# Kernel optimization log

Hardware: AMD Instinct MI355X
Metric: run time of the kernel (lower is better)

## Reference

```python
import jax, jax.numpy as jnp
import numpy as np

WINDOW = 512  # sliding-window size (keys per query, including self)


def setup_inputs() -> dict:
    key = jax.random.key(0)
    ks = jax.random.split(key, 5)
    B, T, C = 2, 8192, 1024
    s = 1.0 / np.sqrt(C)
    return {
        "x": jax.random.normal(ks[0], (B, T, C), dtype=jnp.float32),
        "Wq": jax.random.normal(ks[1], (C, C), dtype=jnp.float32) * s,
        "Wk": jax.random.normal(ks[2], (C, C), dtype=jnp.float32) * s,
        "Wv": jax.random.normal(ks[3], (C, C), dtype=jnp.float32) * s,
        "Wo": jax.random.normal(ks[4], (C, C), dtype=jnp.float32) * s,
    }


def _block_local_attn(q, k, v, window):
    # q,k,v: [B,H,T,D]; causal sliding-window attention, honoring sparsity by
    # attending only to the current and previous block of size `window`.
    B, H, T, D = q.shape
    W = window
    nb = T // W
    scale = 1.0 / jnp.sqrt(jnp.asarray(D, q.dtype))
    qb = q.reshape(B, H, nb, W, D)
    kb = k.reshape(B, H, nb, W, D)
    vb = v.reshape(B, H, nb, W, D)
    # previous block (zero-padded for block 0)
    kp = jnp.pad(kb, ((0, 0), (0, 0), (1, 0), (0, 0), (0, 0)))[:, :, :nb]
    vp = jnp.pad(vb, ((0, 0), (0, 0), (1, 0), (0, 0), (0, 0)))[:, :, :nb]
    k2 = jnp.concatenate([kp, kb], axis=3)  # [B,H,nb,2W,D]
    v2 = jnp.concatenate([vp, vb], axis=3)
    i = jnp.arange(W)[:, None]          # query index within block
    j = jnp.arange(2 * W)[None, :]      # key index (0..W-1 prev, W..2W-1 cur)
    # key global offset = j - W relative to query block start; causal window of
    # size W (self + W-1 previous) <=> i < j <= i + W
    base = (j > i) & (j <= i + W)                                  # [W,2W]
    prev_ok = (jnp.arange(nb)[:, None] > 0) | (jnp.arange(2 * W)[None, :] >= W)
    mask = base[None, :, :] & prev_ok[:, None, :]                  # [nb,W,2W]
    scores = jnp.einsum("bhnqd,bhnkd->bhnqk", qb, k2) * scale
    scores = jnp.where(mask[None, None], scores, jnp.asarray(-1e30, scores.dtype))
    p = jax.nn.softmax(scores, axis=-1)
    out = jnp.einsum("bhnqk,bhnkd->bhnqd", p, v2)
    return out.reshape(B, H, T, D)


def reference(x, Wq, Wk, Wv, Wo):
    B, T, C = x.shape
    H = 16
    D = C // H
    # nn.Linear(y = x @ W^T), bias=False
    q = (x @ Wq.T).reshape(B, T, H, D).transpose(0, 2, 1, 3)
    k = (x @ Wk.T).reshape(B, T, H, D).transpose(0, 2, 1, 3)
    v = (x @ Wv.T).reshape(B, T, H, D).transpose(0, 2, 1, 3)
    out = _block_local_attn(q, k, v, WINDOW)
    out = out.transpose(0, 2, 1, 3).reshape(B, T, C)
    return out @ Wo.T
```

## Files before the change

kernel.cpp:

```cpp
#include <hip/hip_runtime.h>
#include <hip/hip_bf16.h>
#include <stdint.h>

typedef __attribute__((ext_vector_type(8))) short short8;
typedef __attribute__((ext_vector_type(4))) float f32x4;
typedef __hip_bfloat16 bf16;

#define AS1 __attribute__((address_space(1)))
#define AS3 __attribute__((address_space(3)))

__device__ __forceinline__ void gl16(const void* g, void* l) {
  __builtin_amdgcn_global_load_lds((const AS1 unsigned int*)g,
                                   (AS3 unsigned int*)l, 16, 0, 0);
}

__device__ __forceinline__ unsigned short bfbits(float x) {
  union { bf16 b; unsigned short u; } c; c.b = __float2bfloat16(x); return c.u;
}

#define SCHED0 __builtin_amdgcn_sched_barrier(0)

__global__ __launch_bounds__(256) void k_cvt(const float* __restrict__ src,
                                             bf16* __restrict__ dst, int n8) {
  int i = blockIdx.x * blockDim.x + threadIdx.x;
  int stride = gridDim.x * blockDim.x;
  for (; i < n8; i += stride) {
    const float4* p = (const float4*)src + (size_t)i * 2;
    float4 a = p[0], b = p[1];
    bf16 tmp[8];
    tmp[0] = __float2bfloat16(a.x); tmp[1] = __float2bfloat16(a.y);
    tmp[2] = __float2bfloat16(a.z); tmp[3] = __float2bfloat16(a.w);
    tmp[4] = __float2bfloat16(b.x); tmp[5] = __float2bfloat16(b.y);
    tmp[6] = __float2bfloat16(b.z); tmp[7] = __float2bfloat16(b.w);
    *(short8*)(dst + (size_t)i * 8) = *(short8*)tmp;
  }
}


#define GEMM_BODY(...)                                                         \
  const int Kd = 1024;                                                         \
  const int nk = 32;                                              \
  __shared__ bf16 As[4][256 * 32];                                             \
  __shared__ bf16 Bs[4][256 * 32];                                             \
  int tid = threadIdx.x;                                                       \
  int lane = tid & 63, wid = tid >> 6;                                         \
  int l15 = lane & 15, hi = lane >> 4;                                         \
  int wm = wid >> 2, wn = wid & 3;                                             \
  f32x4 acc[8][4];                                                             \
  _Pragma("unroll") for (int i = 0; i < 8; i++)                                \
      _Pragma("unroll") for (int j = 0; j < 4; j++)                            \
          acc[i][j] = (f32x4){0.f, 0.f, 0.f, 0.f};                             \
  auto stageA = [&](int slot, int kk) {                                        \
    const bf16* ab = Abase + kk * 32;                                          \
    _Pragma("unroll") for (int pass = 0; pass < 2; pass++) {                   \
      int p = pass * 512 + tid;                                                \
      int row = p >> 2;                                                        \
      int u = (p & 3) ^ ((row >> 1) & 3);                                      \
      gl16(ab + (size_t)row * Kd + u * 8, (char*)(&As[slot][0]) + p * 16);     \
    }                                                                          \
  };                                                                           \
  auto stageB = [&](int slot, int kk) {                                        \
    const bf16* bb = Bbase + kk * 32;                                          \
    _Pragma("unroll") for (int pass = 0; pass < 2; pass++) {                   \
      int p = pass * 512 + tid;                                                \
      int row = p >> 2;                                                        \
      int u = (p & 3) ^ ((row >> 1) & 3);                                      \
      gl16(bb + (size_t)row * Kd + u * 8, (char*)(&Bs[slot][0]) + p * 16);     \
    }                                                                          \
  };                                                                           \
  stageA(0, 0); stageB(0, 0);                                                  \
  stageA(1, 1); stageB(1, 1);                                                  \
  stageA(2, 2); stageB(2, 2);                                                  \
  asm volatile("s_waitcnt vmcnt(8)" ::: "memory");                             \
  SCHED0; __builtin_amdgcn_s_barrier(); SCHED0;                                \
  int sw = ((l15 >> 1) & 3) << 4;                                              \
  for (int t = 0; t < nk; ++t) {                                               \
    int slot = t & 3;                                                          \
    const char* Ab = (const char*)(&As[slot][0]);                              \
    const char* Bb = (const char*)(&Bs[slot][0]);                              \
             \
    if (t + 3 < nk) stageA((t + 3) & 3, t + 3);                                \
    short8 afr[4], bfr[4];                                                     \
    _Pragma("unroll") for (int mf = 0; mf < 4; mf++) {                         \
      int row = wm * 128 + mf * 16 + l15;                                      \
      afr[mf] = *(const short8*)(Ab + ((row * 64 + hi * 16) ^ sw));            \
    }                                                                          \
    _Pragma("unroll") for (int nf = 0; nf < 4; nf++) {                         \
      int row = wn * 64 + nf * 16 + l15;                                       \
      bfr[nf] = *(const short8*)(Bb + ((row * 64 + hi * 16) ^ sw));            \
    }                                                                          \
    SCHED0; __builtin_amdgcn_s_barrier(); SCHED0;                              \
    __builtin_amdgcn_s_setprio(1);                                             \
    _Pragma("unroll") for (int mf = 0; mf < 4; mf++)                           \
        _Pragma("unroll") for (int nf = 0; nf < 4; nf++)                       \
            acc[mf][nf] = __builtin_amdgcn_mfma_f32_16x16x32_bf16(             \
                afr[mf], bfr[nf], acc[mf][nf], 0, 0, 0);                       \
    __builtin_amdgcn_s_setprio(0);                                             \
    SCHED0; __builtin_amdgcn_s_barrier(); SCHED0;                              \
                  \
    if (t + 3 < nk) stageB((t + 3) & 3, t + 3);                                \
    short8 afr2[4];                                                            \
    _Pragma("unroll") for (int mf = 0; mf < 4; mf++) {                         \
      int row = wm * 128 + 64 + mf * 16 + l15;                                 \
      afr2[mf] = *(const short8*)(Ab + ((row * 64 + hi * 16) ^ sw));           \
    }                                                                          \
    SCHED0;                                                                    \
    if (t + 3 < nk)      asm volatile("s_waitcnt vmcnt(8)" ::: "memory");      \
    else if (t + 2 < nk) asm volatile("s_waitcnt vmcnt(4)" ::: "memory");      \
    else if (t + 1 < nk) asm volatile("s_waitcnt vmcnt(0)" ::: "memory");      \
    SCHED0; __builtin_amdgcn_s_barrier(); SCHED0;                              \
    __builtin_amdgcn_s_setprio(1);                                             \
    _Pragma("unroll") for (int mf = 0; mf < 4; mf++)                           \
        _Pragma("unroll") for (int nf = 0; nf < 4; nf++)                       \
            acc[mf + 4][nf] = __builtin_amdgcn_mfma_f32_16x16x32_bf16(         \
                afr2[mf], bfr[nf], acc[mf + 4][nf], 0, 0, 0);                  \
    __builtin_amdgcn_s_setprio(0);                                             \
    if (t + 1 < nk) { SCHED0; __builtin_amdgcn_s_barrier(); SCHED0; }          \
  }                                                                            \
  __VA_ARGS__

__global__ __launch_bounds__(512, 2) void k_qkv_gemm(
    const bf16* __restrict__ X, const bf16* __restrict__ Wq,
    const bf16* __restrict__ Wk, const bf16* __restrict__ Wv,
    bf16* __restrict__ Q, bf16* __restrict__ K, bf16* __restrict__ V) {
  int bid = blockIdx.x;
  int wsel = bid >> 8;
  int rem = bid & 255;
  int mt = rem & 63;
  int nt = rem >> 6;
  const bf16* W = (wsel == 0) ? Wq : (wsel == 1) ? Wk : Wv;
  bf16* Dst = (wsel == 0) ? Q : (wsel == 1) ? K : V;
  const bf16* Abase = X + (size_t)mt * 256 * 1024;
  const bf16* Bbase = W + (size_t)nt * 256 * 1024;
  GEMM_BODY({
    _Pragma("unroll") for (int mf = 0; mf < 8; mf++) {
      _Pragma("unroll") for (int r = 0; r < 4; r++) {
        int row = mt * 256 + wm * 128 + mf * 16 + hi * 4 + r;
        int b = row >> 13;
        int tok = row & 8191;
        _Pragma("unroll") for (int nf = 0; nf < 4; nf++) {
          int col = nt * 256 + wn * 64 + nf * 16 + l15;
          int h = col >> 6;
          int d = col & 63;
          Dst[((size_t)(b * 16 + h) * 8192 + tok) * 64 + d] =
              __float2bfloat16(acc[mf][nf][r]);
        }
      }
    }
  })
}

__global__ __launch_bounds__(512, 2) void k_out_gemm(
    const bf16* __restrict__ A, const bf16* __restrict__ Wo,
    float* __restrict__ Out) {
  int bid = blockIdx.x;
  int mt = bid & 63;
  int nt = bid >> 6;
  const bf16* Abase = A + (size_t)mt * 256 * 1024;
  const bf16* Bbase = Wo + (size_t)nt * 256 * 1024;
  GEMM_BODY({
    _Pragma("unroll") for (int mf = 0; mf < 8; mf++) {
      _Pragma("unroll") for (int r = 0; r < 4; r++) {
        int row = mt * 256 + wm * 128 + mf * 16 + hi * 4 + r;
        _Pragma("unroll") for (int nf = 0; nf < 4; nf++) {
          int col = nt * 256 + wn * 64 + nf * 16 + l15;
          Out[(size_t)row * 1024 + col] = acc[mf][nf][r];
        }
      }
    }
  })
}

__global__ __launch_bounds__(256) void k_vtrans(const bf16* __restrict__ V,
                                                bf16* __restrict__ VT) {
  const int T = 8192;
  __shared__ bf16 tile[64][72];
  int bid = blockIdx.x;
  int tb = bid & 127;
  int bh = bid >> 7;
  int t0 = tb * 64;
  int tid = threadIdx.x;
  int r = tid >> 2, c4 = tid & 3;
  const bf16* src = V + ((size_t)bh * T + t0 + r) * 64 + c4 * 16;
  short8 a = *(const short8*)src;
  short8 b2 = *(const short8*)(src + 8);
#pragma unroll
  for (int e = 0; e < 8; e++) tile[r][c4 * 16 + e] = ((bf16*)&a)[e];
#pragma unroll
  for (int e = 0; e < 8; e++) tile[r][c4 * 16 + 8 + e] = ((bf16*)&b2)[e];
  __syncthreads();
  alignas(16) bf16 o[16];
#pragma unroll
  for (int e = 0; e < 16; e++) o[e] = tile[c4 * 16 + e][r];
  bf16* dst = VT + ((size_t)bh * 64 + r) * T + t0 + c4 * 16;
  *(short8*)dst = *(short8*)o;
  *(short8*)(dst + 8) = *((short8*)o + 1);
}

__global__ __launch_bounds__(256) void k_attn(
    const bf16* __restrict__ Q, const bf16* __restrict__ K,
    const bf16* __restrict__ VT, bf16* __restrict__ ATT) {
  const int T = 8192;
  __shared__ bf16 Ks[2][64 * 64];
  __shared__ bf16 Vs[2][64 * 64];
  __shared__ bf16 Ps[4][16 * 64];
  int bid = blockIdx.x;
  int qt = bid & 127;
  int bh = bid >> 7;
  int b = bh >> 4, h = bh & 15;
  int tid = threadIdx.x;
  int lane = tid & 63, wid = tid >> 6;
  int l15 = lane & 15, hi = lane >> 4;
  int q0 = qt * 64;
  int qw = q0 + wid * 16;

  short8 bq[2];
  const bf16* qp = Q + ((size_t)bh * T + qw + l15) * 64 + hi * 8;
  bq[0] = *(const short8*)qp;
  bq[1] = *(const short8*)(qp + 32);

  const bf16* Kbh = K + (size_t)bh * T * 64;
  const bf16* Vbh = VT + (size_t)bh * 64 * T;

  auto stage = [&](int bb, int c0) {
#pragma unroll
    for (int pass = 0; pass < 2; pass++) {
      int p = pass * 256 + tid;
      int row = p >> 3;
      int u = (p & 7) ^ (row & 7);
      gl16(Kbh + ((size_t)(c0 + row)) * 64 + u * 8, (char*)(&Ks[bb][0]) + p * 16);
      gl16(Vbh + (size_t)row * T + c0 + u * 8, (char*)(&Vs[bb][0]) + p * 16);
    }
  };

  int cstart = q0 - 512; if (cstart < 0) cstart = 0;
  int nch = (q0 + 64 - cstart) >> 6;

  f32x4 oacc[4];
#pragma unroll
  for (int c = 0; c < 4; c++) oacc[c] = (f32x4){0.f, 0.f, 0.f, 0.f};
  float m = -1e30f, ssum = 0.f;

  stage(0, cstart);
  __syncthreads();
  int buf = 0;
  for (int ci = 0; ci < nch; ci++) {
    int c0 = cstart + (ci << 6);
    if (ci + 1 < nch) stage(buf ^ 1, c0 + 64);
    f32x4 sacc[4];
#pragma unroll
    for (int ks = 0; ks < 4; ks++) sacc[ks] = (f32x4){0.f, 0.f, 0.f, 0.f};
#pragma unroll
    for (int dh = 0; dh < 2; dh++) {
#pragma unroll
      for (int ks = 0; ks < 4; ks++) {
        int krow = ks * 16 + l15;
        int boff = ((krow * 64 + dh * 32 + hi * 8) * 2) ^ ((krow & 7) << 4);
        short8 ak = *(const short8*)((const char*)(&Ks[buf][0]) + boff);
        sacc[ks] = __builtin_amdgcn_mfma_f32_16x16x32_bf16(ak, bq[dh], sacc[ks], 0, 0, 0);
      }
    }
    int qg = qw + l15;
    float pv[4][4];
    float pmax = -1e30f;
#pragma unroll
    for (int ks = 0; ks < 4; ks++)
#pragma unroll
      for (int r = 0; r < 4; r++) {
        int jg = c0 + ks * 16 + hi * 4 + r;
        float s = sacc[ks][r] * 0.125f;
        bool ok = (jg <= qg) && (jg > qg - 512);
        s = ok ? s : -1e30f;
        pv[ks][r] = s;
        pmax = fmaxf(pmax, s);
      }
    pmax = fmaxf(pmax, __shfl_xor(pmax, 16));
    pmax = fmaxf(pmax, __shfl_xor(pmax, 32));
    float mnew = fmaxf(m, pmax);
    float corr = __expf(m - mnew);
    float psum = 0.f;
#pragma unroll
    for (int ks = 0; ks < 4; ks++)
#pragma unroll
      for (int r = 0; r < 4; r++) {
        float p = (pv[ks][r] > -1e29f) ? __expf(pv[ks][r] - mnew) : 0.f;
        pv[ks][r] = p;
        psum += p;
      }
    psum += __shfl_xor(psum, 16);
    psum += __shfl_xor(psum, 32);
    ssum = ssum * corr + psum;
    m = mnew;
#pragma unroll
    for (int r = 0; r < 4; r++) {
      float f = __shfl(corr, hi * 4 + r);
#pragma unroll
      for (int c = 0; c < 4; c++) oacc[c][r] *= f;
    }
#pragma unroll
    for (int ks = 0; ks < 4; ks++) {
      unsigned int lo = (unsigned)bfbits(pv[ks][0]) | ((unsigned)bfbits(pv[ks][1]) << 16);
      unsigned int hi2 = (unsigned)bfbits(pv[ks][2]) | ((unsigned)bfbits(pv[ks][3]) << 16);
      int j0 = ks * 16 + hi * 4;
      int a0 = ((l15 * 64 + j0) * 2) ^ ((l15 & 7) << 4);
      int a1 = ((l15 * 64 + j0 + 2) * 2) ^ ((l15 & 7) << 4);
      *(unsigned int*)((char*)(&Ps[wid][0]) + a0) = lo;
      *(unsigned int*)((char*)(&Ps[wid][0]) + a1) = hi2;
    }
    short8 ap[2];
#pragma unroll
    for (int js = 0; js < 2; js++) {
      int a = ((l15 * 64 + js * 32 + hi * 8) * 2) ^ ((l15 & 7) << 4);
      ap[js] = *(const short8*)((const char*)(&Ps[wid][0]) + a);
    }
#pragma unroll
    for (int js = 0; js < 2; js++)
#pragma unroll
      for (int c = 0; c < 4; c++) {
        int vrow = c * 16 + l15;
        int boff = ((vrow * 64 + js * 32 + hi * 8) * 2) ^ ((vrow & 7) << 4);
        short8 bv = *(const short8*)((const char*)(&Vs[buf][0]) + boff);
        oacc[c] = __builtin_amdgcn_mfma_f32_16x16x32_bf16(ap[js], bv, oacc[c], 0, 0, 0);
      }
    __syncthreads();
    buf ^= 1;
  }
  float inv = 1.f / ssum;
#pragma unroll
  for (int r = 0; r < 4; r++) {
    float f = __shfl(inv, hi * 4 + r);
    int tok = qw + hi * 4 + r;
    bf16* dst = ATT + ((size_t)b * 8192 + tok) * 1024 + h * 64;
#pragma unroll
    for (int c = 0; c < 4; c++)
      dst[c * 16 + l15] = __float2bfloat16(oacc[c][r] * f);
  }
}

extern "C" void kernel_launch(void* const* d_in, const int* in_sizes, int n_in,
                              void* d_out, int out_size, void* d_ws, size_t ws_size,
                              hipStream_t stream) {
  const float* x  = (const float*)d_in[0];
  const float* wq = (const float*)d_in[1];
  const float* wk = (const float*)d_in[2];
  const float* wv = (const float*)d_in[3];
  const float* wo = (const float*)d_in[4];
  float* out = (float*)d_out;

  char* ws = (char*)d_ws;
  const size_t SZ_X = (size_t)16384 * 1024 * 2;
  const size_t SZ_W = (size_t)1024 * 1024 * 2;
  size_t off = 0;
  bf16* xb  = (bf16*)(ws + off); off += SZ_X;
  bf16* wqb = (bf16*)(ws + off); off += SZ_W;
  bf16* wkb = (bf16*)(ws + off); off += SZ_W;
  bf16* wvb = (bf16*)(ws + off); off += SZ_W;
  bf16* wob = (bf16*)(ws + off); off += SZ_W;
  bf16* qb  = (bf16*)(ws + off); off += SZ_X;
  bf16* kb  = (bf16*)(ws + off); off += SZ_X;
  bf16* vb  = (bf16*)(ws + off); off += SZ_X;
  bf16* vtb = (bf16*)(ws + off); off += SZ_X;
  bf16* att = xb;

  k_cvt<<<2048, 256, 0, stream>>>(x, xb, 16384 * 1024 / 8);
  k_cvt<<<512, 256, 0, stream>>>(wq, wqb, 1024 * 1024 / 8);
  k_cvt<<<512, 256, 0, stream>>>(wk, wkb, 1024 * 1024 / 8);
  k_cvt<<<512, 256, 0, stream>>>(wv, wvb, 1024 * 1024 / 8);
  k_cvt<<<512, 256, 0, stream>>>(wo, wob, 1024 * 1024 / 8);
  k_qkv_gemm<<<768, 512, 0, stream>>>(xb, wqb, wkb, wvb, qb, kb, vb);
  k_vtrans<<<4096, 256, 0, stream>>>(vb, vtb);
  k_attn<<<4096, 256, 0, stream>>>(qb, kb, vtb, att);
  k_out_gemm<<<256, 512, 0, stream>>>(att, wob, out);
}
```

Baseline: 327.5 us.

## Software-pipeline LDS fragment loads in GEMM main loop, cut barriers per iteration

Restructures the GEMM k-loop so A and B fragments for the next k-step are read from LDS while the current step's second MFMA half is issued, with register double-buffering of the B fragments. The per-iteration barrier count drops from four to two, and the loop is unrolled by two. The aim is to hide LDS read latency behind MFMA work and cut synchronisation stalls. The cost is higher register pressure from the extra fragment buffers, which could hurt occupancy under launch_bounds(512,2). It also relies on subtle correctness of slot reuse with fewer barriers.

```diff
diff --git a/kernel.cpp b/kernel.cpp
--- a/kernel.cpp
+++ b/kernel.cpp
@@ -74,48 +74,58 @@
   asm volatile("s_waitcnt vmcnt(8)" ::: "memory");                             \
   SCHED0; __builtin_amdgcn_s_barrier(); SCHED0;                                \
   int sw = ((l15 >> 1) & 3) << 4;                                              \
-  for (int t = 0; t < nk; ++t) {                                               \
+  int arow0 = wm * 128 + l15;                                                  \
+  int brow0 = wn * 64 + l15;                                                   \
+  short8 a_cur[4], a_hi[4], b_cur[4], b_nxt[4];                                \
+  _Pragma("unroll") for (int mf = 0; mf < 4; mf++)                             \
+      a_cur[mf] = *(const short8*)((const char*)(&As[0][0]) +                  \
+                                   (((arow0 + mf * 16) * 64 + hi * 16) ^ sw)); \
+  _Pragma("unroll") for (int nf = 0; nf < 4; nf++)                             \
+      b_cur[nf] = *(const short8*)((const char*)(&Bs[0][0]) +                  \
+                                   (((brow0 + nf * 16) * 64 + hi * 16) ^ sw)); \
+  _Pragma("unroll 2") for (int t = 0; t < nk; ++t) {                           \
     int slot = t & 3;                                                          \
     const char* Ab = (const char*)(&As[slot][0]);                              \
-    const char* Bb = (const char*)(&Bs[slot][0]);                              \
              \
     if (t + 3 < nk) stageA((t + 3) & 3, t + 3);                                \
-    short8 afr[4], bfr[4];                                                     \
-    _Pragma("unroll") for (int mf = 0; mf < 4; mf++) {                         \
-      int row = wm * 128 + mf * 16 + l15;                                      \
-      afr[mf] = *(const short8*)(Ab + ((row * 64 + hi * 16) ^ sw));            \
-    }                                                                          \
-    _Pragma("unroll") for (int nf = 0; nf < 4; nf++) {                         \
-      int row = wn * 64 + nf * 16 + l15;                                       \
-      bfr[nf] = *(const short8*)(Bb + ((row * 64 + hi * 16) ^ sw));            \
-    }                                                                          \
-    SCHED0; __builtin_amdgcn_s_barrier(); SCHED0;                              \
+    _Pragma("unroll") for (int mf = 0; mf < 4; mf++)                           \
+        a_hi[mf] = *(const short8*)(Ab +                                       \
+            (((arow0 + 64 + mf * 16) * 64 + hi * 16) ^ sw));                   \
+    SCHED0;                                                                    \
     __builtin_amdgcn_s_setprio(1);                                             \
     _Pragma("unroll") for (int mf = 0; mf < 4; mf++)                           \
         _Pragma("unroll") for (int nf = 0; nf < 4; nf++)                       \
             acc[mf][nf] = __builtin_amdgcn_mfma_f32_16x16x32_bf16(             \
-                afr[mf], bfr[nf], acc[mf][nf], 0, 0, 0);                       \
+                a_cur[mf], b_cur[nf], acc[mf][nf], 0, 0, 0);                   \
     __builtin_amdgcn_s_setprio(0);                                             \
-    SCHED0; __builtin_amdgcn_s_barrier(); SCHED0;                              \
-                  \
+    SCHED0;                                                                    \
+      \
     if (t + 3 < nk) stageB((t + 3) & 3, t + 3);                                \
-    short8 afr2[4];                                                            \
-    _Pragma("unroll") for (int mf = 0; mf < 4; mf++) {                         \
-      int row = wm * 128 + 64 + mf * 16 + l15;                                 \
-      afr2[mf] = *(const short8*)(Ab + ((row * 64 + hi * 16) ^ sw));           \
+    if (t + 1 < nk) {                                                          \
+      SCHED0;                                                                  \
+      if (t + 3 < nk)      asm volatile("s_waitcnt vmcnt(8)" ::: "memory");    \
+      else if (t + 2 < nk) asm volatile("s_waitcnt vmcnt(4)" ::: "memory");    \
+      else                 asm volatile("s_waitcnt vmcnt(0)" ::: "memory");    \
+      SCHED0; __builtin_amdgcn_s_barrier(); SCHED0;                            \
+      const char* AbN = (const char*)(&As[(t + 1) & 3][0]);                    \
+      const char* BbN = (const char*)(&Bs[(t + 1) & 3][0]);                    \
+      _Pragma("unroll") for (int mf = 0; mf < 4; mf++)                         \
+          a_cur[mf] = *(const short8*)(AbN +                                   \
+              (((arow0 + mf * 16) * 64 + hi * 16) ^ sw));                      \
+      _Pragma("unroll") for (int nf = 0; nf < 4; nf++)                         \
+          b_nxt[nf] = *(const short8*)(BbN +                                   \
+              (((brow0 + nf * 16) * 64 + hi * 16) ^ sw));                      \
+      SCHED0;                                                                  \
     }                                                                          \
-    SCHED0;                                                                    \
-    if (t + 3 < nk)      asm volatile("s_waitcnt vmcnt(8)" ::: "memory");      \
-    else if (t + 2 < nk) asm volatile("s_waitcnt vmcnt(4)" ::: "memory");      \
-    else if (t + 1 < nk) asm volatile("s_waitcnt vmcnt(0)" ::: "memory");      \
-    SCHED0; __builtin_amdgcn_s_barrier(); SCHED0;                              \
     __builtin_amdgcn_s_setprio(1);                                             \
     _Pragma("unroll") for (int mf = 0; mf < 4; mf++)                           \
         _Pragma("unroll") for (int nf = 0; nf < 4; nf++)                       \
             acc[mf + 4][nf] = __builtin_amdgcn_mfma_f32_16x16x32_bf16(         \
-                afr2[mf], bfr[nf], acc[mf + 4][nf], 0, 0, 0);                  \
+                a_hi[mf], b_cur[nf], acc[mf + 4][nf], 0, 0, 0);                \
     __builtin_amdgcn_s_setprio(0);                                             \
-    if (t + 1 < nk) { SCHED0; __builtin_amdgcn_s_barrier(); SCHED0; }          \
+    SCHED0;                                                                    \
+    if (t + 1 < nk) { __builtin_amdgcn_s_barrier(); SCHED0; }                  \
+    _Pragma("unroll") for (int nf = 0; nf < 4; nf++) b_cur[nf] = b_nxt[nf];    \
   }                                                                            \
   __VA_ARGS__
 
```

New measurement: 310.4 us. 1.06x faster.
